# Kernel optimization log

Measured on AMD Instinct MI355X. Metric: run time of the kernel, lower is better.

## Reference

```python
import jax, jax.numpy as jnp
import numpy as np

N_NODES = 100000
N_EDGES = 1600000
D_IN = 128
D_HID = 128
D_OUT = 128


def _sage_conv(x, src, dst, W_l, b_l, W_r, num_nodes):
    # PyG SAGEConv (aggr='mean'): out = lin_l(mean_{j in N(i)} x_j) + lin_r(x_i)
    msg = x[src]  # [E, d] gather source features
    agg = jax.ops.segment_sum(msg, dst, num_segments=num_nodes)  # [N, d]
    deg = jax.ops.segment_sum(jnp.ones((src.shape[0],), x.dtype), dst, num_segments=num_nodes)
    mean = agg / jnp.maximum(deg, 1.0)[:, None]
    return mean @ W_l.T + b_l + x @ W_r.T


def setup_inputs() -> dict:
    key = jax.random.key(0)
    ks = jax.random.split(key, 8)
    x = jax.random.normal(ks[0], (N_NODES, D_IN), dtype=jnp.float32)
    edge_index = jax.random.randint(ks[1], (2, N_EDGES), 0, N_NODES, dtype=jnp.int64)
    s = 1.0 / np.sqrt(D_IN)
    W_l1 = jax.random.uniform(ks[2], (D_HID, D_IN), jnp.float32, -s, s)
    b_l1 = jnp.zeros((D_HID,), jnp.float32)
    W_r1 = jax.random.uniform(ks[3], (D_HID, D_IN), jnp.float32, -s, s)
    s2 = 1.0 / np.sqrt(D_HID)
    W_l2 = jax.random.uniform(ks[4], (D_OUT, D_HID), jnp.float32, -s2, s2)
    b_l2 = jnp.zeros((D_OUT,), jnp.float32)
    W_r2 = jax.random.uniform(ks[5], (D_OUT, D_HID), jnp.float32, -s2, s2)
    return {"x": x, "edge_index": edge_index, "W_l1": W_l1, "b_l1": b_l1,
            "W_r1": W_r1, "W_l2": W_l2, "b_l2": b_l2, "W_r2": W_r2}


def reference(x, edge_index, W_l1, b_l1, W_r1, W_l2, b_l2, W_r2):
    src, dst = edge_index[0], edge_index[1]
    n = x.shape[0]
    h = _sage_conv(x, src, dst, W_l1, b_l1, W_r1, n)
    h = jax.nn.relu(h)
    out = _sage_conv(h, src, dst, W_l2, b_l2, W_r2, n)
    return out
```

## Files before the change

kernel.cpp:

```cpp
#include <hip/hip_runtime.h>
#include <stdint.h>

typedef short bf16x8 __attribute__((ext_vector_type(8)));
typedef float f32x4 __attribute__((ext_vector_type(4)));

#define NPB 512
#define BSHIFT 9
#define MAXBUCK 256
#define STAGE_CAP 12288

__device__ __forceinline__ short f2bf(float f) {
    uint32_t u = __float_as_uint(f);
    u += 0x7fffu + ((u >> 16) & 1u);
    return (short)(u >> 16);
}
__device__ __forceinline__ float bf2f(unsigned short s) {
    return __uint_as_float((uint32_t)s << 16);
}

__global__ __launch_bounds__(256) void convx_kernel(const float* __restrict__ in,
                                                    short* __restrict__ out, int n) {
    int i = (blockIdx.x * 256 + threadIdx.x) * 8;
    if (i + 8 <= n) {
        const float4 v0 = *(const float4*)(in + i);
        const float4 v1 = *(const float4*)(in + i + 4);
        bf16x8 o;
        o[0] = f2bf(v0.x); o[1] = f2bf(v0.y); o[2] = f2bf(v0.z); o[3] = f2bf(v0.w);
        o[4] = f2bf(v1.x); o[5] = f2bf(v1.y); o[6] = f2bf(v1.z); o[7] = f2bf(v1.w);
        *(bf16x8*)(out + i) = o;
    } else {
        for (int j = i; j < n; ++j) out[j] = f2bf(in[j]);
    }
}

__global__ void convw4_kernel(const float* __restrict__ w0, const float* __restrict__ w1,
                              const float* __restrict__ w2, const float* __restrict__ w3,
                              short* __restrict__ o0, short* __restrict__ o1,
                              short* __restrict__ o2, short* __restrict__ o3) {
    int i = blockIdx.x * 256 + threadIdx.x;
    o0[i] = f2bf(w0[i]);
    o1[i] = f2bf(w1[i]);
    o2[i] = f2bf(w2[i]);
    o3[i] = f2bf(w3[i]);
}

__global__ __launch_bounds__(256) void bhist_kernel(const int* __restrict__ dst,
                                                    int* __restrict__ bcnt, int E, int B) {
    __shared__ int h[MAXBUCK];
    for (int i = threadIdx.x; i < B; i += 256) h[i] = 0;
    __syncthreads();
    int stride = gridDim.x * 256;
    for (int e = blockIdx.x * 256 + threadIdx.x; e < E; e += stride)
        atomicAdd(&h[dst[e] >> BSHIFT], 1);
    __syncthreads();
    for (int i = threadIdx.x; i < B; i += 256)
        if (h[i]) atomicAdd(&bcnt[i], h[i]);
}

__global__ __launch_bounds__(256) void bscan_kernel(const int* __restrict__ bcnt,
                                                    int* __restrict__ bbase,
                                                    int* __restrict__ gcur,
                                                    int* __restrict__ rowptr,
                                                    int E, int N, int B) {
    __shared__ int s[256];
    int t = threadIdx.x;
    int v = (t < B) ? bcnt[t] : 0;
    s[t] = v;
    __syncthreads();
    for (int off = 1; off < 256; off <<= 1) {
        int a = (t >= off) ? s[t - off] : 0;
        __syncthreads();
        s[t] += a;
        __syncthreads();
    }
    int excl = s[t] - v;
    if (t < B) { bbase[t] = excl; gcur[t] = excl; }
    if (t == B - 1) bbase[B] = excl + v;
    if (t == 0) rowptr[N] = E;
}

__global__ __launch_bounds__(256) void bin_kernel(const int* __restrict__ src,
                                                  const int* __restrict__ dst,
                                                  int* __restrict__ gcur,
                                                  unsigned int* __restrict__ binned,
                                                  int E, int B) {
    __shared__ int cnt[MAXBUCK];
    __shared__ int base[MAXBUCK];
    for (int i = threadIdx.x; i < B; i += 256) cnt[i] = 0;
    __syncthreads();
    const int e0 = blockIdx.x * 4096;
    int myS[16], myD[16];
    int n = 0;
#pragma unroll
    for (int i = 0; i < 16; ++i) {
        int e = e0 + threadIdx.x + i * 256;
        if (e < E) { myS[n] = src[e]; myD[n] = dst[e]; ++n; }
    }
    for (int i = 0; i < n; ++i) atomicAdd(&cnt[myD[i] >> BSHIFT], 1);
    __syncthreads();
    for (int i = threadIdx.x; i < B; i += 256) {
        int c = cnt[i];
        base[i] = c ? atomicAdd(&gcur[i], c) : 0;
        cnt[i] = 0;
    }
    __syncthreads();
    for (int i = 0; i < n; ++i) {
        int b = myD[i] >> BSHIFT;
        int off = atomicAdd(&cnt[b], 1);
        binned[base[b] + off] = ((unsigned)myS[i] << BSHIFT) | (unsigned)(myD[i] & (NPB - 1));
    }
}

__global__ __launch_bounds__(256) void build_kernel(const unsigned int* __restrict__ binned,
                                                    const int* __restrict__ bbase,
                                                    int* __restrict__ rowptr,
                                                    int* __restrict__ csr, int N) {
    __shared__ int hist[NPB];
    __shared__ int cur[NPB];
    __shared__ int scanb[256];
    __shared__ int stage[STAGE_CAP];
    const int b = blockIdx.x;
    const int t = threadIdx.x;
    const int cbeg = bbase[b], cend = bbase[b + 1];
    const int cnt = cend - cbeg;
    for (int i = t; i < NPB; i += 256) hist[i] = 0;
    __syncthreads();
    for (int i = t; i < cnt; i += 256)
        atomicAdd(&hist[binned[cbeg + i] & (NPB - 1)], 1);
    __syncthreads();
    const int h0 = hist[2 * t], h1 = hist[2 * t + 1];
    const int ps = h0 + h1;
    scanb[t] = ps;
    __syncthreads();
    for (int off = 1; off < 256; off <<= 1) {
        int a = (t >= off) ? scanb[t - off] : 0;
        __syncthreads();
        scanb[t] += a;
        __syncthreads();
    }
    const int e0 = scanb[t] - ps;
    cur[2 * t]     = e0;
    cur[2 * t + 1] = e0 + h0;
    __syncthreads();
    const int node0 = b << BSHIFT;
    for (int i = t; i < NPB; i += 256) {
        int node = node0 + i;
        if (node < N) rowptr[node] = cbeg + cur[i];
    }
    __syncthreads();
    for (int i = t; i < cnt; i += 256) {
        unsigned rec = binned[cbeg + i];
        int ld  = rec & (NPB - 1);
        int pos = atomicAdd(&cur[ld], 1);
        if (pos < STAGE_CAP) stage[pos] = (int)(rec >> BSHIFT);
        else                 csr[cbeg + pos] = (int)(rec >> BSHIFT);
    }
    __syncthreads();
    const int lim = cnt < STAGE_CAP ? cnt : STAGE_CAP;
    for (int i = t; i < lim; i += 256)
        csr[cbeg + i] = stage[i];
}

__global__ __launch_bounds__(256) void agg_kernel(
    const short* __restrict__ feat, const int* __restrict__ csr,
    const int* __restrict__ rowptr, short* __restrict__ mean, int N) {
    int node = blockIdx.x * 4 + (threadIdx.x >> 6);
    if (node >= N) return;
    const int lane = threadIdx.x & 63;
    const int half = lane >> 5;
    const int c4   = (lane & 31) * 4;
    const int beg = rowptr[node], end = rowptr[node + 1];
    float a0 = 0.f, a1 = 0.f, a2 = 0.f, a3 = 0.f;
    int e = beg;
    for (; e + 4 <= end; e += 4) {
        int sa = csr[e + half];
        int sb = csr[e + 2 + half];
        ushort4 ua = *(const ushort4*)(feat + (size_t)sa * 128 + c4);
        ushort4 ub = *(const ushort4*)(feat + (size_t)sb * 128 + c4);
        a0 += bf2f(ua.x) + bf2f(ub.x);
        a1 += bf2f(ua.y) + bf2f(ub.y);
        a2 += bf2f(ua.z) + bf2f(ub.z);
        a3 += bf2f(ua.w) + bf2f(ub.w);
    }
    for (; e + 2 <= end; e += 2) {
        int s = csr[e + half];
        ushort4 u = *(const ushort4*)(feat + (size_t)s * 128 + c4);
        a0 += bf2f(u.x); a1 += bf2f(u.y); a2 += bf2f(u.z); a3 += bf2f(u.w);
    }
    if (e < end && half == 0) {
        int s = csr[e];
        ushort4 u = *(const ushort4*)(feat + (size_t)s * 128 + c4);
        a0 += bf2f(u.x); a1 += bf2f(u.y); a2 += bf2f(u.z); a3 += bf2f(u.w);
    }
    a0 += __shfl_xor(a0, 32);
    a1 += __shfl_xor(a1, 32);
    a2 += __shfl_xor(a2, 32);
    a3 += __shfl_xor(a3, 32);
    if (half == 0) {
        float r = 1.0f / fmaxf((float)(end - beg), 1.0f);
        ushort4 o;
        o.x = (unsigned short)f2bf(a0 * r);
        o.y = (unsigned short)f2bf(a1 * r);
        o.z = (unsigned short)f2bf(a2 * r);
        o.w = (unsigned short)f2bf(a3 * r);
        *(ushort4*)(mean + (size_t)node * 128 + c4) = o;
    }
}

template <bool RELU>
__global__ __launch_bounds__(256) void gemm_kernel(
    const short* __restrict__ mean, const short* __restrict__ xin,
    const short* __restrict__ Wl, const short* __restrict__ Wr,
    const float* __restrict__ bias,
    short* __restrict__ outb, float* __restrict__ outf, int N)
{
    const int lane = threadIdx.x & 63;
    const int wave = threadIdx.x >> 6;
    const int m0   = blockIdx.x * 64 + wave * 16;
    const int mrow = m0 + (lane & 15);
    const int kq   = (lane >> 4) * 8;
    const bool valid = (mrow < N);

    f32x4 acc[8];
#pragma unroll
    for (int i = 0; i < 8; ++i) acc[i] = (f32x4)0.0f;

#pragma unroll
    for (int kk = 0; kk < 4; ++kk) {
        const int kb = kk * 32 + kq;
        bf16x8 a = (bf16x8)0;
        if (valid) a = *(const bf16x8*)(mean + (size_t)mrow * 128 + kb);
#pragma unroll
        for (int nt = 0; nt < 8; ++nt) {
            const bf16x8 b = *(const bf16x8*)(Wl + (size_t)(nt * 16 + (lane & 15)) * 128 + kb);
            acc[nt] = __builtin_amdgcn_mfma_f32_16x16x32_bf16(a, b, acc[nt], 0, 0, 0);
        }
    }
#pragma unroll
    for (int kk = 0; kk < 4; ++kk) {
        const int kb = kk * 32 + kq;
        bf16x8 a = (bf16x8)0;
        if (valid) a = *(const bf16x8*)(xin + (size_t)mrow * 128 + kb);
#pragma unroll
        for (int nt = 0; nt < 8; ++nt) {
            const bf16x8 b = *(const bf16x8*)(Wr + (size_t)(nt * 16 + (lane & 15)) * 128 + kb);
            acc[nt] = __builtin_amdgcn_mfma_f32_16x16x32_bf16(a, b, acc[nt], 0, 0, 0);
        }
    }

    const int col0  = lane & 15;
    const int rbase = m0 + (lane >> 4) * 4;
#pragma unroll
    for (int nt = 0; nt < 8; ++nt) {
        const int col = nt * 16 + col0;
        const float bc = bias[col];
#pragma unroll
        for (int r = 0; r < 4; ++r) {
            const int node = rbase + r;
            if (node < N) {
                float v = acc[nt][r] + bc;
                if (RELU) outb[(size_t)node * 128 + col] = f2bf(fmaxf(v, 0.0f));
                else      outf[(size_t)node * 128 + col] = v;
            }
        }
    }
}

extern "C" void kernel_launch(void* const* d_in, const int* in_sizes, int n_in,
                              void* d_out, int out_size, void* d_ws, size_t ws_size,
                              hipStream_t stream) {
    const float* x   = (const float*)d_in[0];
    const int*   ei  = (const int*)d_in[1];
    const float* Wl1 = (const float*)d_in[2];
    const float* bl1 = (const float*)d_in[3];
    const float* Wr1 = (const float*)d_in[4];
    const float* Wl2 = (const float*)d_in[5];
    const float* bl2 = (const float*)d_in[6];
    const float* Wr2 = (const float*)d_in[7];

    const int N = in_sizes[0] / 128;
    const int E = in_sizes[1] / 2;
    const int* src = ei;
    const int* dst = ei + E;
    const int B = (N + NPB - 1) >> BSHIFT;

    short* hbuf = (short*)d_ws;
    short* mean = hbuf + (size_t)N * 128;
    short* wl1  = mean + (size_t)N * 128;
    short* wr1  = wl1 + 16384;
    short* wl2  = wr1 + 16384;
    short* wr2  = wl2 + 16384;

    char* ob = (char*)d_out;
    short* xb = (short*)ob;
    size_t off = (size_t)N * 128 * 2;
    int* rowptr = (int*)(ob + off);
    off += ((size_t)(N + 1) * 4 + 15) & ~(size_t)15;
    int* csr = (int*)(ob + off);
    off += ((size_t)E * 4 + 15) & ~(size_t)15;
    unsigned int* binned = (unsigned int*)(ob + off);
    off += ((size_t)E * 4 + 15) & ~(size_t)15;
    int* bcnt  = (int*)(ob + off);
    int* bbase = bcnt + (MAXBUCK + 1);
    int* gcur  = bbase + (MAXBUCK + 1);
    float* out = (float*)d_out;

    const int aggBlocks  = (N + 3) / 4;
    const int gemmBlocks = (N + 63) / 64;
    const int binBlocks  = (E + 4095) / 4096;

    convx_kernel<<<(N * 128 / 8 + 255) / 256, 256, 0, stream>>>(x, xb, N * 128);
    convw4_kernel<<<64, 256, 0, stream>>>(Wl1, Wr1, Wl2, Wr2, wl1, wr1, wl2, wr2);

    (void)hipMemsetAsync(bcnt, 0, (size_t)(MAXBUCK + 1) * sizeof(int), stream);
    bhist_kernel<<<256, 256, 0, stream>>>(dst, bcnt, E, B);
    bscan_kernel<<<1, 256, 0, stream>>>(bcnt, bbase, gcur, rowptr, E, N, B);
    bin_kernel<<<binBlocks, 256, 0, stream>>>(src, dst, gcur, binned, E, B);
    build_kernel<<<B, 256, 0, stream>>>(binned, bbase, rowptr, csr, N);

    agg_kernel<<<aggBlocks, 256, 0, stream>>>(xb, csr, rowptr, mean, N);
    gemm_kernel<true><<<gemmBlocks, 256, 0, stream>>>(mean, xb, wl1, wr1, bl1,
                                                      hbuf, (float*)nullptr, N);
    agg_kernel<<<aggBlocks, 256, 0, stream>>>(hbuf, csr, rowptr, mean, N);
    gemm_kernel<false><<<gemmBlocks, 256, 0, stream>>>(mean, hbuf, wl2, wr2, bl2,
                                                       (short*)nullptr, out, N);
}
```

Measured before the change: 466.1 us.

## Fuse neighbor mean aggregation into the MFMA GEMM through LDS staging

Merges the separate aggregation and GEMM kernels into one kernel per layer. Each wave computes the neighbor means for its 16 rows, using 16-byte gathers per lane and four rows at a time, and writes them to padded LDS rows. The MFMA GEMM then reads its A operand from LDS, which removes the global write and re-read of the mean buffer in both layers. The CSR and rowptr scratch moves from the output buffer to the workspace. The trade-off is fewer waves per node during gathering, so there may be less memory-level parallelism on the irregular gather, and GEMM issue now waits on the gather phase.

```diff
diff --git a/kernel.cpp b/kernel.cpp
--- a/kernel.cpp
+++ b/kernel.cpp
@@ -2,12 +2,14 @@
 #include <stdint.h>
 
 typedef short bf16x8 __attribute__((ext_vector_type(8)));
+typedef unsigned short u16x8 __attribute__((ext_vector_type(8)));
 typedef float f32x4 __attribute__((ext_vector_type(4)));
 
 #define NPB 512
 #define BSHIFT 9
 #define MAXBUCK 256
 #define STAGE_CAP 12288
+#define LROW 136
 
 __device__ __forceinline__ short f2bf(float f) {
     uint32_t u = __float_as_uint(f);
@@ -161,98 +163,86 @@
         csr[cbeg + i] = stage[i];
 }
 
-__global__ __launch_bounds__(256) void agg_kernel(
+template <bool RELU>
+__global__ __launch_bounds__(256) void fused_kernel(
     const short* __restrict__ feat, const int* __restrict__ csr,
-    const int* __restrict__ rowptr, short* __restrict__ mean, int N) {
-    int node = blockIdx.x * 4 + (threadIdx.x >> 6);
-    if (node >= N) return;
-    const int lane = threadIdx.x & 63;
-    const int half = lane >> 5;
-    const int c4   = (lane & 31) * 4;
-    const int beg = rowptr[node], end = rowptr[node + 1];
-    float a0 = 0.f, a1 = 0.f, a2 = 0.f, a3 = 0.f;
-    int e = beg;
-    for (; e + 4 <= end; e += 4) {
-        int sa = csr[e + half];
-        int sb = csr[e + 2 + half];
-        ushort4 ua = *(const ushort4*)(feat + (size_t)sa * 128 + c4);
-        ushort4 ub = *(const ushort4*)(feat + (size_t)sb * 128 + c4);
-        a0 += bf2f(ua.x) + bf2f(ub.x);
-        a1 += bf2f(ua.y) + bf2f(ub.y);
-        a2 += bf2f(ua.z) + bf2f(ub.z);
-        a3 += bf2f(ua.w) + bf2f(ub.w);
-    }
-    for (; e + 2 <= end; e += 2) {
-        int s = csr[e + half];
-        ushort4 u = *(const ushort4*)(feat + (size_t)s * 128 + c4);
-        a0 += bf2f(u.x); a1 += bf2f(u.y); a2 += bf2f(u.z); a3 += bf2f(u.w);
-    }
-    if (e < end && half == 0) {
-        int s = csr[e];
-        ushort4 u = *(const ushort4*)(feat + (size_t)s * 128 + c4);
-        a0 += bf2f(u.x); a1 += bf2f(u.y); a2 += bf2f(u.z); a3 += bf2f(u.w);
-    }
-    a0 += __shfl_xor(a0, 32);
-    a1 += __shfl_xor(a1, 32);
-    a2 += __shfl_xor(a2, 32);
-    a3 += __shfl_xor(a3, 32);
-    if (half == 0) {
-        float r = 1.0f / fmaxf((float)(end - beg), 1.0f);
-        ushort4 o;
-        o.x = (unsigned short)f2bf(a0 * r);
-        o.y = (unsigned short)f2bf(a1 * r);
-        o.z = (unsigned short)f2bf(a2 * r);
-        o.w = (unsigned short)f2bf(a3 * r);
-        *(ushort4*)(mean + (size_t)node * 128 + c4) = o;
-    }
-}
-
-template <bool RELU>
-__global__ __launch_bounds__(256) void gemm_kernel(
-    const short* __restrict__ mean, const short* __restrict__ xin,
+    const int* __restrict__ rowptr,
     const short* __restrict__ Wl, const short* __restrict__ Wr,
     const float* __restrict__ bias,
     short* __restrict__ outb, float* __restrict__ outf, int N)
 {
+    __shared__ short lmean[64 * LROW];
     const int lane = threadIdx.x & 63;
     const int wave = threadIdx.x >> 6;
+    const int q    = lane >> 4;
+    const int ql   = lane & 15;
     const int m0   = blockIdx.x * 64 + wave * 16;
-    const int mrow = m0 + (lane & 15);
-    const int kq   = (lane >> 4) * 8;
-    const bool valid = (mrow < N);
+
+    for (int it = 0; it < 4; ++it) {
+        const int node = m0 + it * 4 + q;
+        float a0=0,a1=0,a2=0,a3=0,a4=0,a5=0,a6=0,a7=0;
+        if (node < N) {
+            const int beg = rowptr[node], end = rowptr[node + 1];
+            int e = beg;
+            for (; e + 4 <= end; e += 4) {
+                const int s0 = csr[e], s1 = csr[e+1], s2 = csr[e+2], s3 = csr[e+3];
+                u16x8 u0 = *(const u16x8*)(feat + (size_t)s0 * 128 + ql * 8);
+                u16x8 u1 = *(const u16x8*)(feat + (size_t)s1 * 128 + ql * 8);
+                u16x8 u2 = *(const u16x8*)(feat + (size_t)s2 * 128 + ql * 8);
+                u16x8 u3 = *(const u16x8*)(feat + (size_t)s3 * 128 + ql * 8);
+                a0 += bf2f(u0[0]) + bf2f(u1[0]) + bf2f(u2[0]) + bf2f(u3[0]);
+                a1 += bf2f(u0[1]) + bf2f(u1[1]) + bf2f(u2[1]) + bf2f(u3[1]);
+                a2 += bf2f(u0[2]) + bf2f(u1[2]) + bf2f(u2[2]) + bf2f(u3[2]);
+                a3 += bf2f(u0[3]) + bf2f(u1[3]) + bf2f(u2[3]) + bf2f(u3[3]);
+                a4 += bf2f(u0[4]) + bf2f(u1[4]) + bf2f(u2[4]) + bf2f(u3[4]);
+                a5 += bf2f(u0[5]) + bf2f(u1[5]) + bf2f(u2[5]) + bf2f(u3[5]);
+                a6 += bf2f(u0[6]) + bf2f(u1[6]) + bf2f(u2[6]) + bf2f(u3[6]);
+                a7 += bf2f(u0[7]) + bf2f(u1[7]) + bf2f(u2[7]) + bf2f(u3[7]);
+            }
+            for (; e < end; ++e) {
+                u16x8 u = *(const u16x8*)(feat + (size_t)csr[e] * 128 + ql * 8);
+                a0 += bf2f(u[0]); a1 += bf2f(u[1]); a2 += bf2f(u[2]); a3 += bf2f(u[3]);
+                a4 += bf2f(u[4]); a5 += bf2f(u[5]); a6 += bf2f(u[6]); a7 += bf2f(u[7]);
+            }
+            const float r = 1.0f / fmaxf((float)(end - beg), 1.0f);
+            bf16x8 o;
+            o[0] = f2bf(a0 * r); o[1] = f2bf(a1 * r); o[2] = f2bf(a2 * r); o[3] = f2bf(a3 * r);
+            o[4] = f2bf(a4 * r); o[5] = f2bf(a5 * r); o[6] = f2bf(a6 * r); o[7] = f2bf(a7 * r);
+            *(bf16x8*)(lmean + (size_t)(wave * 16 + it * 4 + q) * LROW + ql * 8) = o;
+        }
+    }
 
     f32x4 acc[8];
 #pragma unroll
     for (int i = 0; i < 8; ++i) acc[i] = (f32x4)0.0f;
+    const bool valid = (m0 + ql < N);
 
 #pragma unroll
     for (int kk = 0; kk < 4; ++kk) {
-        const int kb = kk * 32 + kq;
-        bf16x8 a = (bf16x8)0;
-        if (valid) a = *(const bf16x8*)(mean + (size_t)mrow * 128 + kb);
+        const int kb = kk * 32 + q * 8;
+        const bf16x8 a = *(const bf16x8*)(lmean + (size_t)(wave * 16 + ql) * LROW + kb);
 #pragma unroll
         for (int nt = 0; nt < 8; ++nt) {
-            const bf16x8 b = *(const bf16x8*)(Wl + (size_t)(nt * 16 + (lane & 15)) * 128 + kb);
+            const bf16x8 b = *(const bf16x8*)(Wl + (size_t)(nt * 16 + ql) * 128 + kb);
             acc[nt] = __builtin_amdgcn_mfma_f32_16x16x32_bf16(a, b, acc[nt], 0, 0, 0);
         }
     }
 #pragma unroll
     for (int kk = 0; kk < 4; ++kk) {
-        const int kb = kk * 32 + kq;
+        const int kb = kk * 32 + q * 8;
         bf16x8 a = (bf16x8)0;
-        if (valid) a = *(const bf16x8*)(xin + (size_t)mrow * 128 + kb);
+        if (valid) a = *(const bf16x8*)(feat + (size_t)(m0 + ql) * 128 + kb);
 #pragma unroll
         for (int nt = 0; nt < 8; ++nt) {
-            const bf16x8 b = *(const bf16x8*)(Wr + (size_t)(nt * 16 + (lane & 15)) * 128 + kb);
+            const bf16x8 b = *(const bf16x8*)(Wr + (size_t)(nt * 16 + ql) * 128 + kb);
             acc[nt] = __builtin_amdgcn_mfma_f32_16x16x32_bf16(a, b, acc[nt], 0, 0, 0);
         }
     }
 
-    const int col0  = lane & 15;
-    const int rbase = m0 + (lane >> 4) * 4;
+    const int rbase = m0 + q * 4;
 #pragma unroll
     for (int nt = 0; nt < 8; ++nt) {
-        const int col = nt * 16 + col0;
+        const int col = nt * 16 + ql;
         const float bc = bias[col];
 #pragma unroll
         for (int r = 0; r < 4; ++r) {
@@ -284,30 +274,28 @@
     const int* dst = ei + E;
     const int B = (N + NPB - 1) >> BSHIFT;
 
-    short* hbuf = (short*)d_ws;
-    short* mean = hbuf + (size_t)N * 128;
-    short* wl1  = mean + (size_t)N * 128;
-    short* wr1  = wl1 + 16384;
-    short* wl2  = wr1 + 16384;
-    short* wr2  = wl2 + 16384;
-
-    char* ob = (char*)d_out;
-    short* xb = (short*)ob;
+    char* wsb = (char*)d_ws;
+    short* hbuf = (short*)wsb;
     size_t off = (size_t)N * 128 * 2;
-    int* rowptr = (int*)(ob + off);
+    short* wl1 = (short*)(wsb + off); off += 16384 * 2;
+    short* wr1 = (short*)(wsb + off); off += 16384 * 2;
+    short* wl2 = (short*)(wsb + off); off += 16384 * 2;
+    short* wr2 = (short*)(wsb + off); off += 16384 * 2;
+    int* rowptr = (int*)(wsb + off);
     off += ((size_t)(N + 1) * 4 + 15) & ~(size_t)15;
-    int* csr = (int*)(ob + off);
+    int* csr = (int*)(wsb + off);
     off += ((size_t)E * 4 + 15) & ~(size_t)15;
-    unsigned int* binned = (unsigned int*)(ob + off);
+    unsigned int* binned = (unsigned int*)(wsb + off);
     off += ((size_t)E * 4 + 15) & ~(size_t)15;
-    int* bcnt  = (int*)(ob + off);
+    int* bcnt  = (int*)(wsb + off);
     int* bbase = bcnt + (MAXBUCK + 1);
     int* gcur  = bbase + (MAXBUCK + 1);
+
+    short* xb  = (short*)d_out;
     float* out = (float*)d_out;
 
-    const int aggBlocks  = (N + 3) / 4;
-    const int gemmBlocks = (N + 63) / 64;
-    const int binBlocks  = (E + 4095) / 4096;
+    const int fusedBlocks = (N + 63) / 64;
+    const int binBlocks   = (E + 4095) / 4096;
 
     convx_kernel<<<(N * 128 / 8 + 255) / 256, 256, 0, stream>>>(x, xb, N * 128);
     convw4_kernel<<<64, 256, 0, stream>>>(Wl1, Wr1, Wl2, Wr2, wl1, wr1, wl2, wr2);
@@ -318,10 +306,8 @@
     bin_kernel<<<binBlocks, 256, 0, stream>>>(src, dst, gcur, binned, E, B);
     build_kernel<<<B, 256, 0, stream>>>(binned, bbase, rowptr, csr, N);
 
-    agg_kernel<<<aggBlocks, 256, 0, stream>>>(xb, csr, rowptr, mean, N);
-    gemm_kernel<true><<<gemmBlocks, 256, 0, stream>>>(mean, xb, wl1, wr1, bl1,
-                                                      hbuf, (float*)nullptr, N);
-    agg_kernel<<<aggBlocks, 256, 0, stream>>>(hbuf, csr, rowptr, mean, N);
-    gemm_kernel<false><<<gemmBlocks, 256, 0, stream>>>(mean, hbuf, wl2, wr2, bl2,
-                                                       (short*)nullptr, out, N);
-}
+    fused_kernel<true><<<fusedBlocks, 256, 0, stream>>>(xb, csr, rowptr, wl1, wr1, bl1,
+                                                        hbuf, (float*)nullptr, N);
+    fused_kernel<false><<<fusedBlocks, 256, 0, stream>>>(hbuf, csr, rowptr, wl2, wr2, bl2,
+                                                         (short*)nullptr, out, N);
+}
```

Result: faster. 432.9 us (-7.1%).
